# Kernel tuning notes

Hardware: AMD Instinct MI355X
Metric: run time of the kernel (lower is better)

Reference implementation:

```python
import jax, jax.numpy as jnp
import numpy as np

H = 16  # num_heads

def _toroidal_bias(S, dtype):
    # float mask: +1.0 at (i, (i-1)%S), (i,i), (i, (i+1)%S); PyTorch ADDS float attn_mask to scores
    eye = jnp.eye(S, dtype=dtype)
    return eye + jnp.roll(eye, 1, axis=1) + jnp.roll(eye, -1, axis=1)

def setup_inputs() -> dict:
    key = jax.random.key(0)
    ks = jax.random.split(key, 7)
    E = 1024
    S, B = 2048, 2
    sc = 0.02
    return {
        "x": jax.random.normal(ks[0], (S, B, E), dtype=jnp.float32),
        "w_tor": jax.random.normal(ks[1], (E, E), dtype=jnp.float32) * sc,
        "b_tor": jax.random.normal(ks[2], (E,), dtype=jnp.float32) * sc,
        "in_proj_w": jax.random.normal(ks[3], (3 * E, E), dtype=jnp.float32) * sc,
        "in_proj_b": jax.random.normal(ks[4], (3 * E,), dtype=jnp.float32) * sc,
        "out_w": jax.random.normal(ks[5], (E, E), dtype=jnp.float32) * sc,
        "out_b": jax.random.normal(ks[6], (E,), dtype=jnp.float32) * sc,
    }

def reference(x, w_tor, b_tor, in_proj_w, in_proj_b, out_w, out_b):
    S, B, E = x.shape
    hd = E // H
    scale = 1.0 / jnp.sqrt(jnp.asarray(hd, dtype=x.dtype))
    # toroidal projection, then fused in_proj (self-attention: q=k=v=x_toroidal)
    xt = x @ w_tor.T + b_tor                      # (S,B,E)
    qkv = xt @ in_proj_w.T + in_proj_b            # (S,B,3E)
    q, k, v = jnp.split(qkv, 3, axis=-1)
    def to_heads(t):
        return t.reshape(S, B, H, hd).transpose(1, 2, 0, 3)  # (B,H,S,hd)
    q, k, v = to_heads(q), to_heads(k), to_heads(v)
    bias = _toroidal_bias(S, x.dtype)             # (S,S) additive float mask
    scores = jnp.einsum('bhqd,bhkd->bhqk', q * scale, k) + bias
    attn = jax.nn.softmax(scores, axis=-1)
    o = jnp.einsum('bhqk,bhkd->bhqd', attn, v)    # (B,H,S,hd)
    o = o.transpose(2, 0, 1, 3).reshape(S, B, E)
    return o @ out_w.T + out_b
```

## Files before the change

### kernel.cpp

```cpp
#include <hip/hip_runtime.h>

#define S_LEN 2048
#define NB    2
#define EMB   1024
#define NH    16
#define HD    64

typedef __bf16 bf16_t;
typedef bf16_t bf16x8 __attribute__((ext_vector_type(8)));
typedef bf16_t bf16x4v __attribute__((ext_vector_type(4)));
typedef float  f32x4  __attribute__((ext_vector_type(4)));
typedef float  f32x16 __attribute__((ext_vector_type(16)));

#define L2E 1.44269504f

__device__ __forceinline__ void g2l16(const void* g, void* l) {
    auto gp = reinterpret_cast<const unsigned int __attribute__((address_space(1)))*>(
        reinterpret_cast<uintptr_t>(g));
    auto lp = reinterpret_cast<unsigned int __attribute__((address_space(3)))*>(
        reinterpret_cast<uintptr_t>(l));
    __builtin_amdgcn_global_load_lds(gp, lp, 16, 0, 0);
}

__global__ __launch_bounds__(256) void cast4_f32_bf16(
    const float* __restrict__ s0, bf16_t* __restrict__ d0,
    const float* __restrict__ s1, bf16_t* __restrict__ d1,
    const float* __restrict__ s2, bf16_t* __restrict__ d2,
    const float* __restrict__ s3, bf16_t* __restrict__ d3)
{
    long i = (long)blockIdx.x * 256 + threadIdx.x;
    const float* s; bf16_t* d; long off;
    if (i < 1048576)      { s = s0; d = d0; off = i; }
    else if (i < 1310720) { s = s1; d = d1; off = i - 1048576; }
    else if (i < 2097152) { s = s2; d = d2; off = i - 1310720; }
    else                  { s = s3; d = d3; off = i - 2097152; }
    float4 v = ((const float4*)s)[off];
    bf16x4v o;
    o[0] = (bf16_t)v.x; o[1] = (bf16_t)v.y; o[2] = (bf16_t)v.z; o[3] = (bf16_t)v.w;
    *(bf16x4v*)(d + off * 4) = o;
}

template<int TN, int MODE>
__global__ __launch_bounds__(256) void gemm_bt_bf16(
    const bf16_t* __restrict__ A, const bf16_t* __restrict__ W,
    const float* __restrict__ bias, void* __restrict__ Cout,
    bf16_t* __restrict__ Qp, bf16_t* __restrict__ Kp, bf16_t* __restrict__ Vtp,
    int M, int N, int K)
{
    constexpr int MB = (TN == 128) ? 4 : 2;
    __shared__ __align__(16) bf16_t As[2][128 * 32];
    __shared__ __align__(16) bf16_t Bs[2][TN * 32];

    const int tid  = threadIdx.x;
    const int lane = tid & 63;
    const int w    = tid >> 6;
    const int lm   = lane & 15;
    const int lq   = lane >> 4;
    const long m0  = (long)blockIdx.y * 128;
    const long n0  = (long)blockIdx.x * TN;
    const int wm0  = (TN == 128) ? (w >> 1) * 64 : w * 32;
    const int wn0  = (TN == 128) ? (w & 1) * 64 : 0;

    f32x4 acc[MB][4];
#pragma unroll
    for (int i = 0; i < MB; ++i)
#pragma unroll
        for (int j = 0; j < 4; ++j) acc[i][j] = (f32x4){0.f, 0.f, 0.f, 0.f};

    auto stage = [&](int k0, int buf) {
        bf16_t* asb = &As[buf][0];
        bf16_t* bsb = &Bs[buf][0];
#pragma unroll
        for (int j = 0; j < 2; ++j) {
            int a   = (w * 2 + j) * 64 + lane;
            int row = a >> 2;
            int c   = (a & 3) ^ ((row >> 1) & 3);
            g2l16(A + (m0 + row) * K + k0 + c * 8, asb + (w * 2 + j) * 512);
        }
#pragma unroll
        for (int j = 0; j < TN / 64; ++j) {
            int a   = (w * (TN / 64) + j) * 64 + lane;
            int row = a >> 2;
            int c   = (a & 3) ^ ((row >> 1) & 3);
            g2l16(W + (n0 + row) * K + k0 + c * 8, bsb + (w * (TN / 64) + j) * 512);
        }
    };

    stage(0, 0);
    for (int k0 = 0; k0 < K; k0 += 32) {
        const int cur = (k0 >> 5) & 1;
        asm volatile("s_waitcnt vmcnt(0)" ::: "memory");
        __syncthreads();
        if (k0 + 32 < K) stage(k0 + 32, cur ^ 1);

        bf16x8 af[MB], bfr[4];
#pragma unroll
        for (int mb = 0; mb < MB; ++mb) {
            int r = wm0 + mb * 16 + lm;
            af[mb] = *(const bf16x8*)&As[cur][r * 32 + ((lq ^ ((r >> 1) & 3)) << 3)];
        }
#pragma unroll
        for (int nb = 0; nb < 4; ++nb) {
            int r = wn0 + nb * 16 + lm;
            bfr[nb] = *(const bf16x8*)&Bs[cur][r * 32 + ((lq ^ ((r >> 1) & 3)) << 3)];
        }
#pragma unroll
        for (int mb = 0; mb < MB; ++mb)
#pragma unroll
            for (int nb = 0; nb < 4; ++nb)
                acc[mb][nb] = __builtin_amdgcn_mfma_f32_16x16x32_bf16(
                    af[mb], bfr[nb], acc[mb][nb], 0, 0, 0);
    }

    float b4[4];
#pragma unroll
    for (int nb = 0; nb < 4; ++nb) b4[nb] = bias[n0 + wn0 + nb * 16 + lm];

#pragma unroll
    for (int mb = 0; mb < MB; ++mb) {
#pragma unroll
        for (int r = 0; r < 4; ++r) {
            long m = m0 + wm0 + mb * 16 + lq * 4 + r;
#pragma unroll
            for (int nb = 0; nb < 4; ++nb) {
                int n   = (int)n0 + wn0 + nb * 16 + lm;
                float v = acc[mb][nb][r] + b4[nb];
                if (MODE == 0) {
                    ((float*)Cout)[m * N + n] = v;
                } else if (MODE == 1) {
                    ((bf16_t*)Cout)[m * N + n] = (bf16_t)v;
                } else {
                    int sec  = n >> 10;
                    int nloc = n & 1023;
                    int h    = nloc >> 6;
                    int d    = nloc & 63;
                    int s    = (int)(m >> 1), b = (int)(m & 1);
                    int bh   = b * 16 + h;
                    if (sec == 0) {
                        Qp[((size_t)(bh * S_LEN + s)) * 64 + d] =
                            (bf16_t)(v * (0.125f * L2E));
                    } else if (sec == 1) {
                        Kp[((size_t)(bh * S_LEN + s)) * 64 + d] = (bf16_t)v;
                    } else {
                        Vtp[((size_t)(bh * 64 + d)) * S_LEN + s] = (bf16_t)v;
                    }
                }
            }
        }
    }
}

__global__ __launch_bounds__(256, 2) void attn_mfma(
    const bf16_t* __restrict__ Qb, const bf16_t* __restrict__ Kb,
    const bf16_t* __restrict__ Vtb, bf16_t* __restrict__ O)
{
    __shared__ __align__(16) bf16_t Ks[2][8 * 512];
    __shared__ __align__(16) bf16_t Vts[2][8 * 512];
    __shared__ __align__(16) bf16_t Ps[4][8 * 256];

    const int tid  = threadIdx.x;
    const int lane = tid & 63;
    const int w    = tid >> 6;
    const int bh   = blockIdx.x >> 4;
    const int qt   = blockIdx.x & 15;
    const int l5   = lane & 31;
    const int hi   = lane >> 5;

    const bf16_t* qrow = Qb + ((size_t)bh * S_LEN + qt * 128 + w * 32 + l5) * 64 + hi * 8;
    bf16x8 qf[4];
#pragma unroll
    for (int ds = 0; ds < 4; ++ds) qf[ds] = *(const bf16x8*)(qrow + ds * 16);

    f32x16 oacc[2];
#pragma unroll
    for (int dh = 0; dh < 2; ++dh)
#pragma unroll
        for (int i = 0; i < 16; ++i) oacc[dh][i] = 0.f;
    float plsum = 0.f;

    auto stageKV = [&](int kt, int buf) {
        bf16_t* ksb = &Ks[buf][0];
        bf16_t* vsb = &Vts[buf][0];
        const bf16_t* kg = Kb + ((size_t)bh * S_LEN + kt * 64) * 64;
        const bf16_t* vg = Vtb + (size_t)bh * 64 * S_LEN + kt * 64;
#pragma unroll
        for (int j = 0; j < 2; ++j) {
            int c = w * 2 + j;
            g2l16(kg + (size_t)lane * 64 + c * 8,    ksb + c * 512);
            g2l16(vg + (size_t)lane * S_LEN + c * 8, vsb + c * 512);
        }
    };

    stageKV(0, 0);
    for (int kt = 0; kt < 32; ++kt) {
        const int cur = kt & 1;
        asm volatile("s_waitcnt vmcnt(0)" ::: "memory");
        __syncthreads();
        if (kt < 31) stageKV(kt + 1, cur ^ 1);

        f32x16 sacc[2];
#pragma unroll
        for (int kh = 0; kh < 2; ++kh) {
#pragma unroll
            for (int i = 0; i < 16; ++i) sacc[kh][i] = 0.f;
#pragma unroll
            for (int ds = 0; ds < 4; ++ds) {
                bf16x8 kf = *(const bf16x8*)&Ks[cur][(2 * ds + hi) * 512 + (kh * 32 + l5) * 8];
                sacc[kh] = __builtin_amdgcn_mfma_f32_32x32x16_bf16(kf, qf[ds], sacc[kh], 0, 0, 0);
            }
        }

        int ktd = (kt - 2 * qt) & 31;
        if (ktd <= 2 || ktd == 31) {
            int q = qt * 128 + w * 32 + l5;
#pragma unroll
            for (int kh = 0; kh < 2; ++kh)
#pragma unroll
                for (int r = 0; r < 16; ++r) {
                    int key  = kt * 64 + kh * 32 + (r & 3) + 8 * (r >> 2) + 4 * hi;
                    int diff = (key - q) & (S_LEN - 1);
                    if (diff <= 1 || diff == S_LEN - 1) sacc[kh][r] += L2E;
                }
        }

#pragma unroll
        for (int kh = 0; kh < 2; ++kh)
#pragma unroll
            for (int g = 0; g < 4; ++g) {
                bf16x4v pk;
#pragma unroll
                for (int e = 0; e < 4; ++e) {
                    float p = __builtin_amdgcn_exp2f(sacc[kh][g * 4 + e]);
                    plsum += p;
                    pk[e] = (bf16_t)p;
                }
                *(bf16x4v*)&Ps[w][(kh * 4 + g) * 256 + l5 * 8 + hi * 4] = pk;
            }

        bf16x8 pf[4];
#pragma unroll
        for (int ks = 0; ks < 4; ++ks)
            pf[ks] = *(const bf16x8*)&Ps[w][(2 * ks + hi) * 256 + l5 * 8];
#pragma unroll
        for (int dh = 0; dh < 2; ++dh) {
#pragma unroll
            for (int ks = 0; ks < 4; ++ks) {
                bf16x8 vf = *(const bf16x8*)&Vts[cur][(2 * ks + hi) * 512 + (dh * 32 + l5) * 8];
                oacc[dh] = __builtin_amdgcn_mfma_f32_32x32x16_bf16(pf[ks], vf, oacc[dh], 0, 0, 0);
            }
        }
    }

    plsum += __shfl_xor(plsum, 32, 64);
    float* Lw = (float*)&Ps[w][0];
    if (hi == 0) Lw[l5] = plsum;

    float inv16[16];
#pragma unroll
    for (int g = 0; g < 4; ++g) {
        f32x4 lv = *(const f32x4*)&Lw[8 * g + 4 * hi];
#pragma unroll
        for (int e = 0; e < 4; ++e) inv16[g * 4 + e] = 1.0f / lv[e];
    }

    const int b = bh >> 4, h = bh & 15;
#pragma unroll
    for (int dh = 0; dh < 2; ++dh)
#pragma unroll
        for (int r = 0; r < 16; ++r) {
            int qrel = (r & 3) + 8 * (r >> 2) + 4 * hi;
            int s = qt * 128 + w * 32 + qrel;
            O[((size_t)(s * NB + b)) * EMB + h * 64 + dh * 32 + l5] =
                (bf16_t)(oacc[dh][r] * inv16[r]);
        }
}

extern "C" void kernel_launch(void* const* d_in, const int* in_sizes, int n_in,
                              void* d_out, int out_size, void* d_ws, size_t ws_size,
                              hipStream_t stream)
{
    const float* x         = (const float*)d_in[0];
    const float* w_tor     = (const float*)d_in[1];
    const float* b_tor     = (const float*)d_in[2];
    const float* in_proj_w = (const float*)d_in[3];
    const float* in_proj_b = (const float*)d_in[4];
    const float* out_w     = (const float*)d_in[5];
    const float* out_b     = (const float*)d_in[6];
    float* out = (float*)d_out;

    const int M = S_LEN * NB;

    char* base = (char*)d_ws;
    bf16_t* xb    = (bf16_t*)(base);
    bf16_t* wtorb = (bf16_t*)(base + ( 8ull << 20));
    bf16_t* ipwb  = (bf16_t*)(base + (10ull << 20));
    bf16_t* outwb = (bf16_t*)(base + (16ull << 20));
    bf16_t* xtb   = (bf16_t*)(base + (18ull << 20));
    bf16_t* Kb    = (bf16_t*)(base + (26ull << 20));
    bf16_t* Vtb   = (bf16_t*)(base + (34ull << 20));
    bf16_t* Qb    = xb;
    bf16_t* Ob    = xtb;

    cast4_f32_bf16<<<dim3(9216), 256, 0, stream>>>(
        x, xb, w_tor, wtorb, in_proj_w, ipwb, out_w, outwb);

    gemm_bt_bf16<64, 1><<<dim3(EMB / 64, M / 128), 256, 0, stream>>>(
        xb, wtorb, b_tor, xtb, nullptr, nullptr, nullptr, M, EMB, EMB);

    gemm_bt_bf16<128, 2><<<dim3(3 * EMB / 128, M / 128), 256, 0, stream>>>(
        xtb, ipwb, in_proj_b, nullptr, Qb, Kb, Vtb, M, 3 * EMB, EMB);

    attn_mfma<<<dim3(32 * 16), 256, 0, stream>>>(Qb, Kb, Vtb, Ob);

    gemm_bt_bf16<64, 0><<<dim3(EMB / 64, M / 128), 256, 0, stream>>>(
        Ob, outwb, out_b, out, nullptr, nullptr, nullptr, M, EMB, EMB);
}
```

Before: 216.1 us.

## Keep softmax probabilities in registers via permlane32 swap, remap blocks, add setprio

Replaces the per-wave LDS round-trip for the softmax probability tile with packed bf16 pairs exchanged between lane halves using v_permlane32_swap, so P feeds the PV MFMA directly from registers. The block-to-(bh, q-tile) mapping is also changed to interleave heads across workgroups, which may change L2/cache locality of K/V. MFMA phases are wrapped in s_setprio to favour matrix issue across waves. This removes LDS writes and reads plus their latency each tile, and depends on the permlane lane layout matching the MFMA A-operand layout.

Result: no change. 218.5 us (+1.1%).

```diff
diff --git a/kernel.cpp b/kernel.cpp
--- a/kernel.cpp
+++ b/kernel.cpp
@@ -20,6 +20,12 @@
     auto lp = reinterpret_cast<unsigned int __attribute__((address_space(3)))*>(
         reinterpret_cast<uintptr_t>(l));
     __builtin_amdgcn_global_load_lds(gp, lp, 16, 0, 0);
+}
+
+__device__ __forceinline__ unsigned int pk2(float a, float b) {
+    union { unsigned int u; bf16_t h[2]; } r;
+    r.h[0] = (bf16_t)a; r.h[1] = (bf16_t)b;
+    return r.u;
 }
 
 __global__ __launch_bounds__(256) void cast4_f32_bf16(
@@ -156,13 +162,14 @@
 {
     __shared__ __align__(16) bf16_t Ks[2][8 * 512];
     __shared__ __align__(16) bf16_t Vts[2][8 * 512];
-    __shared__ __align__(16) bf16_t Ps[4][8 * 256];
+    __shared__ __align__(16) float  Lw4[4][32];
 
     const int tid  = threadIdx.x;
     const int lane = tid & 63;
     const int w    = tid >> 6;
-    const int bh   = blockIdx.x >> 4;
-    const int qt   = blockIdx.x & 15;
+    const int wg   = blockIdx.x;
+    const int bh   = ((wg & 7) << 2) | (wg >> 7);
+    const int qt   = (wg >> 3) & 15;
     const int l5   = lane & 31;
     const int hi   = lane >> 5;
 
@@ -199,6 +206,7 @@
         if (kt < 31) stageKV(kt + 1, cur ^ 1);
 
         f32x16 sacc[2];
+        __builtin_amdgcn_s_setprio(1);
 #pragma unroll
         for (int kh = 0; kh < 2; ++kh) {
 #pragma unroll
@@ -209,6 +217,7 @@
                 sacc[kh] = __builtin_amdgcn_mfma_f32_32x32x16_bf16(kf, qf[ds], sacc[kh], 0, 0, 0);
             }
         }
+        __builtin_amdgcn_s_setprio(0);
 
         int ktd = (kt - 2 * qt) & 31;
         if (ktd <= 2 || ktd == 31) {
@@ -223,24 +232,34 @@
                 }
         }
 
+        unsigned int Wp[2][4][2];
 #pragma unroll
         for (int kh = 0; kh < 2; ++kh)
 #pragma unroll
             for (int g = 0; g < 4; ++g) {
-                bf16x4v pk;
-#pragma unroll
-                for (int e = 0; e < 4; ++e) {
-                    float p = __builtin_amdgcn_exp2f(sacc[kh][g * 4 + e]);
-                    plsum += p;
-                    pk[e] = (bf16_t)p;
-                }
-                *(bf16x4v*)&Ps[w][(kh * 4 + g) * 256 + l5 * 8 + hi * 4] = pk;
+                float p0 = __builtin_amdgcn_exp2f(sacc[kh][g * 4 + 0]);
+                float p1 = __builtin_amdgcn_exp2f(sacc[kh][g * 4 + 1]);
+                float p2 = __builtin_amdgcn_exp2f(sacc[kh][g * 4 + 2]);
+                float p3 = __builtin_amdgcn_exp2f(sacc[kh][g * 4 + 3]);
+                plsum += (p0 + p1) + (p2 + p3);
+                Wp[kh][g][0] = pk2(p0, p1);
+                Wp[kh][g][1] = pk2(p2, p3);
             }
 
         bf16x8 pf[4];
 #pragma unroll
-        for (int ks = 0; ks < 4; ++ks)
-            pf[ks] = *(const bf16x8*)&Ps[w][(2 * ks + hi) * 256 + l5 * 8];
+        for (int ks = 0; ks < 4; ++ks) {
+            const int kh = ks >> 1, m = ks & 1;
+            unsigned int a0 = Wp[kh][2 * m][0],     a1 = Wp[kh][2 * m][1];
+            unsigned int b0 = Wp[kh][2 * m + 1][0], b1 = Wp[kh][2 * m + 1][1];
+            asm("v_permlane32_swap_b32 %0, %1" : "+v"(a0), "+v"(b0));
+            asm("v_permlane32_swap_b32 %0, %1" : "+v"(a1), "+v"(b1));
+            union { unsigned int u[4]; bf16x8 v; } cv;
+            cv.u[0] = a0; cv.u[1] = a1; cv.u[2] = b0; cv.u[3] = b1;
+            pf[ks] = cv.v;
+        }
+
+        __builtin_amdgcn_s_setprio(1);
 #pragma unroll
         for (int dh = 0; dh < 2; ++dh) {
 #pragma unroll
@@ -249,16 +268,16 @@
                 oacc[dh] = __builtin_amdgcn_mfma_f32_32x32x16_bf16(pf[ks], vf, oacc[dh], 0, 0, 0);
             }
         }
+        __builtin_amdgcn_s_setprio(0);
     }
 
     plsum += __shfl_xor(plsum, 32, 64);
-    float* Lw = (float*)&Ps[w][0];
-    if (hi == 0) Lw[l5] = plsum;
+    if (hi == 0) Lw4[w][l5] = plsum;
 
     float inv16[16];
 #pragma unroll
     for (int g = 0; g < 4; ++g) {
-        f32x4 lv = *(const f32x4*)&Lw[8 * g + 4 * hi];
+        f32x4 lv = *(const f32x4*)&Lw4[w][8 * g + 4 * hi];
 #pragma unroll
         for (int e = 0; e < 4; ++e) inv16[g * 4 + e] = 1.0f / lv[e];
     }
```

## Swizzle K/V LDS layout, remap block order, split P stores, add MFMA priority

Applied to the files above, without the earlier changes.

The attention kernel now stages K and V into LDS with row-major rows and XOR-swizzled 16-byte chunks, and the MFMA operand reads use matching swizzled offsets. This is meant to cut LDS bank conflicts and make global loads more contiguous. The P scratch layout is split into two 4-element halves so stores and loads avoid conflicts. Blocks are also remapped so neighbouring blocks hit different batch-heads, and s_setprio raises wave priority around the MFMA loops. The extra index math and split P loads add a few instructions per tile.

New measurement: 212.1 us. Within noise of the previous version (-1.9%).

```diff
diff --git a/kernel.cpp b/kernel.cpp
--- a/kernel.cpp
+++ b/kernel.cpp
@@ -161,10 +161,17 @@
     const int tid  = threadIdx.x;
     const int lane = tid & 63;
     const int w    = tid >> 6;
-    const int bh   = blockIdx.x >> 4;
-    const int qt   = blockIdx.x & 15;
+    const int bid  = blockIdx.x;
+    const int bh   = ((bid & 7) << 2) | (bid >> 7);
+    const int qt   = (bid >> 3) & 15;
     const int l5   = lane & 31;
     const int hi   = lane >> 5;
+
+    const int rsub = lane >> 3;
+    const int csw  = (lane & 7) ^ rsub;
+    int cc[4];
+#pragma unroll
+    for (int i = 0; i < 4; ++i) cc[i] = ((2 * i + hi) ^ (l5 & 7)) * 8;
 
     const bf16_t* qrow = Qb + ((size_t)bh * S_LEN + qt * 128 + w * 32 + l5) * 64 + hi * 8;
     bf16x8 qf[4];
@@ -185,9 +192,9 @@
         const bf16_t* vg = Vtb + (size_t)bh * 64 * S_LEN + kt * 64;
 #pragma unroll
         for (int j = 0; j < 2; ++j) {
-            int c = w * 2 + j;
-            g2l16(kg + (size_t)lane * 64 + c * 8,    ksb + c * 512);
-            g2l16(vg + (size_t)lane * S_LEN + c * 8, vsb + c * 512);
+            int i = w * 2 + j;
+            g2l16(kg + (size_t)(i * 8 + rsub) * 64 + csw * 8,    ksb + i * 512);
+            g2l16(vg + (size_t)(i * 8 + rsub) * S_LEN + csw * 8, vsb + i * 512);
         }
     };
 
@@ -199,16 +206,18 @@
         if (kt < 31) stageKV(kt + 1, cur ^ 1);
 
         f32x16 sacc[2];
+        __builtin_amdgcn_s_setprio(1);
 #pragma unroll
         for (int kh = 0; kh < 2; ++kh) {
 #pragma unroll
             for (int i = 0; i < 16; ++i) sacc[kh][i] = 0.f;
 #pragma unroll
             for (int ds = 0; ds < 4; ++ds) {
-                bf16x8 kf = *(const bf16x8*)&Ks[cur][(2 * ds + hi) * 512 + (kh * 32 + l5) * 8];
+                bf16x8 kf = *(const bf16x8*)&Ks[cur][(kh * 32 + l5) * 64 + cc[ds]];
                 sacc[kh] = __builtin_amdgcn_mfma_f32_32x32x16_bf16(kf, qf[ds], sacc[kh], 0, 0, 0);
             }
         }
+        __builtin_amdgcn_s_setprio(0);
 
         int ktd = (kt - 2 * qt) & 31;
         if (ktd <= 2 || ktd == 31) {
@@ -234,21 +243,27 @@
                     plsum += p;
                     pk[e] = (bf16_t)p;
                 }
-                *(bf16x4v*)&Ps[w][(kh * 4 + g) * 256 + l5 * 8 + hi * 4] = pk;
+                *(bf16x4v*)&Ps[w][(kh * 4 + g) * 256 + hi * 128 + l5 * 4] = pk;
             }
 
         bf16x8 pf[4];
 #pragma unroll
-        for (int ks = 0; ks < 4; ++ks)
-            pf[ks] = *(const bf16x8*)&Ps[w][(2 * ks + hi) * 256 + l5 * 8];
+        for (int ks = 0; ks < 4; ++ks) {
+            bf16x4v lo = *(const bf16x4v*)&Ps[w][(2 * ks + hi) * 256 + l5 * 4];
+            bf16x4v hb = *(const bf16x4v*)&Ps[w][(2 * ks + hi) * 256 + 128 + l5 * 4];
+#pragma unroll
+            for (int e = 0; e < 4; ++e) { pf[ks][e] = lo[e]; pf[ks][4 + e] = hb[e]; }
+        }
+        __builtin_amdgcn_s_setprio(1);
 #pragma unroll
         for (int dh = 0; dh < 2; ++dh) {
 #pragma unroll
             for (int ks = 0; ks < 4; ++ks) {
-                bf16x8 vf = *(const bf16x8*)&Vts[cur][(2 * ks + hi) * 512 + (dh * 32 + l5) * 8];
+                bf16x8 vf = *(const bf16x8*)&Vts[cur][(dh * 32 + l5) * 64 + cc[ks]];
                 oacc[dh] = __builtin_amdgcn_mfma_f32_32x32x16_bf16(pf[ks], vf, oacc[dh], 0, 0, 0);
             }
         }
+        __builtin_amdgcn_s_setprio(0);
     }
 
     plsum += __shfl_xor(plsum, 32, 64);
```
